# Optimization experiments

Hardware: AMD Instinct MI355X
Metric: run time of the kernel (lower is better)

The kernel has to match this reference:

```python
import jax, jax.numpy as jnp
import numpy as np

B, P, G = 16, 4096, 512          # images, proposals/image, gt boxes/image
NUM_CLASSES = 80
IOU_THRESH = 0.5                  # cfg.MODEL.ROI_HEADS.IOU_THRESHOLDS = [0.5]
BATCH_PER_IMG = 512               # cfg.MODEL.ROI_HEADS.BATCH_SIZE_PER_IMAGE
POS_FRAC = 0.25                   # cfg.MODEL.ROI_HEADS.POSITIVE_FRACTION
NUM_FG = int(BATCH_PER_IMG * POS_FRAC)   # 128
NUM_BG = BATCH_PER_IMG - NUM_FG          # 384
NEG_INF = jnp.float32(-1e9)


def _make_boxes(key, b, n, img_size=1024.0):
    # valid xyxy boxes inside an img_size x img_size image
    p = jax.random.uniform(key, (b, n, 4)) * img_size
    x1 = jnp.minimum(p[..., 0], p[..., 2]); x2 = jnp.maximum(p[..., 0], p[..., 2]) + 1.0
    y1 = jnp.minimum(p[..., 1], p[..., 3]); y2 = jnp.maximum(p[..., 1], p[..., 3]) + 1.0
    return jnp.stack([x1, y1, x2, y2], axis=-1)


def setup_inputs() -> dict:
    key = jax.random.key(0)
    k1, k2, k3, k4 = jax.random.split(key, 4)
    return {
        'proposal_boxes': _make_boxes(k1, B, P),
        'target_boxes': _make_boxes(k2, B, G),
        'gt_classes': jax.random.randint(k3, (B, G), 0, NUM_CLASSES),
        'priorities': jax.random.uniform(k4, (B, P)),  # random sampling keys (replaces tf random subsample)
    }


def _pairwise_iou(t, p):
    # t: [B,G,4] gt boxes, p: [B,P,4] proposals, xyxy -> iou [B,G,P]
    area_t = (t[..., 2] - t[..., 0]) * (t[..., 3] - t[..., 1])   # [B,G]
    area_p = (p[..., 2] - p[..., 0]) * (p[..., 3] - p[..., 1])   # [B,P]
    lt = jnp.maximum(t[:, :, None, :2], p[:, None, :, :2])       # [B,G,P,2]
    rb = jnp.minimum(t[:, :, None, 2:], p[:, None, :, 2:])       # [B,G,P,2]
    wh = jnp.clip(rb - lt, 0.0)
    inter = wh[..., 0] * wh[..., 1]                               # [B,G,P]
    union = area_t[:, :, None] + area_p[:, None, :] - inter
    return jnp.where(inter > 0, inter / jnp.maximum(union, 1e-8), 0.0)


def reference(proposal_boxes, target_boxes, gt_classes, priorities):
    # ---- Matcher: pairwise IoU + argmax over gt (thresholds [0.5], labels [0,1]) ----
    iou = _pairwise_iou(target_boxes, proposal_boxes)       # [B,G,P]
    matched_vals = iou.max(axis=1)                          # [B,P]
    matched_idxs = iou.argmax(axis=1)                       # [B,P]
    fg = matched_vals >= IOU_THRESH                         # label==1
    # gt_classes per proposal: matched class if fg, else background = num_classes
    cls_m = jnp.take_along_axis(gt_classes, matched_idxs, axis=1)
    prop_cls = jnp.where(fg, cls_m, NUM_CLASSES)            # [B,P]
    # ---- subsample_labels: pick up to NUM_FG fg and NUM_BG bg by random priority ----
    fg_sc = jnp.where(fg, priorities, NEG_INF)
    bg_sc = jnp.where(~fg, priorities, NEG_INF)
    fg_v, fg_i = jax.lax.top_k(fg_sc, NUM_FG)               # [B,NUM_FG]
    bg_v, bg_i = jax.lax.top_k(bg_sc, NUM_BG)               # [B,NUM_BG]
    inds = jnp.concatenate([fg_i, bg_i], axis=1)            # [B,S]
    valid = jnp.concatenate([fg_v, bg_v], axis=1) > NEG_INF / 2
    # ---- gather sampled proposals + assigned gt (pad_or_clip: zero invalid slots) ----
    s_boxes = jnp.take_along_axis(proposal_boxes, inds[..., None], axis=1)   # [B,S,4]
    s_midx = jnp.take_along_axis(matched_idxs, inds, axis=1)                  # [B,S]
    s_gt_boxes = jnp.take_along_axis(target_boxes, s_midx[..., None], axis=1) # [B,S,4]
    s_cls = jnp.where(valid, jnp.take_along_axis(prop_cls, inds, axis=1), -1) # [B,S]
    mask = valid[..., None].astype(s_boxes.dtype)
    out = jnp.concatenate([s_boxes, s_gt_boxes], axis=-1) * mask              # [B,S,8]
    return out, s_cls
```

## Files before the change

### kernel.cpp

```cpp
#include <hip/hip_runtime.h>
#include <stdint.h>

#define NB 16
#define NP 4096
#define NG 512
#define NCH 8
#define GC  (NG/NCH)
#define NCLS 80
#define KFG 128
#define KBG 384
#define NS 512
#define OUT_BOX (NB*NS*8)
#define OUT_CLS (NB*NS)
#define NBNP (NB*NP)
#define NBK 256

typedef unsigned long long u64;

__global__ __launch_bounds__(256) void k_match(
    const float4* __restrict__ prop,
    const float4* __restrict__ tgt,
    u64* __restrict__ pm)
{
    __shared__ float4 tb[GC];
    __shared__ float  ta[GC];

    const int tid  = threadIdx.x;
    const int bx   = blockIdx.x;
    const int c    = bx & (NCH - 1);
    const int pblk = (bx >> 3) & 15;
    const int b    = bx >> 7;

    if (tid < GC) {
        float4 t = tgt[b * NG + c * GC + tid];
        tb[tid] = t;
        ta[tid] = __fmul_rn(__fsub_rn(t.z, t.x), __fsub_rn(t.w, t.y));
    }
    __syncthreads();

    const int p = pblk * 256 + tid;
    const float4 pb = prop[b * NP + p];
    const float ap = __fmul_rn(__fsub_rn(pb.z, pb.x), __fsub_rn(pb.w, pb.y));

    float best = -1.0f;
    int   bi   = 0;
    #pragma unroll 4
    for (int g = 0; g < GC; ++g) {
        const float4 t = tb[g];
        const float ltx = fmaxf(t.x, pb.x);
        const float lty = fmaxf(t.y, pb.y);
        const float rbx = fminf(t.z, pb.z);
        const float rby = fminf(t.w, pb.w);
        const float w = fmaxf(__fsub_rn(rbx, ltx), 0.0f);
        const float h = fmaxf(__fsub_rn(rby, lty), 0.0f);
        const float inter = __fmul_rn(w, h);
        const float uni   = __fsub_rn(__fadd_rn(ta[g], ap), inter);
        if ((double)inter > (double)best * (double)uni) {
            const float iou = (inter > 0.0f)
                                ? __fdiv_rn(inter, fmaxf(uni, 1e-8f))
                                : 0.0f;
            if (iou > best) { best = iou; bi = g; }
        }
    }
    const int gg = c * GC + bi;
    pm[c * NBNP + b * NP + p] =
        ((u64)__float_as_uint(best) << 16) | (u64)(NG - 1 - gg);
}

__global__ __launch_bounds__(1024) void k_select(
    const float4* __restrict__ prop,
    const float4* __restrict__ tgt,
    const int*   __restrict__ gtc,
    const float* __restrict__ pri,
    const u64*   __restrict__ pm,
    float* __restrict__ out)
{
    __shared__ int cnt[2 * NBK];
    __shared__ int bsa[2 * NBK];
    __shared__ int cur[2 * NBK];
    __shared__ int sA[2 * NBK], sB[2 * NBK];
    __shared__ int s_tot0;
    __shared__ u64 gkeys[NP];

    const int tid = threadIdx.x;
    const int b   = blockIdx.x;

    float* oimg = out + (size_t)b * NS * 8;
    #pragma unroll
    for (int i = tid; i < NS * 8; i += 1024) oimg[i] = 0.0f;
    if (tid < NS) out[OUT_BOX + b * NS + tid] = -1.0f;

    if (tid < 2 * NBK) cnt[tid] = 0;
    __syncthreads();

    int mcat[4], mgrp[4], mmid[4];
    u64 mkey[4];
    #pragma unroll
    for (int t = 0; t < 4; ++t) {
        const int p = tid + t * 1024;
        const int idx = b * NP + p;
        u64 m = pm[idx];
        #pragma unroll
        for (int c = 1; c < NCH; ++c) {
            const u64 mc = pm[c * NBNP + idx];
            if (mc > m) m = mc;
        }
        const float best = __uint_as_float((unsigned)(m >> 16));
        mmid[t] = (NG - 1) - (int)(m & 0xFFFF);
        const int cat = (best >= 0.5f) ? 1 : 0;
        const float v = pri[idx];
        int bkt = (int)(v * 256.0f); if (bkt > 255) bkt = 255;
        mcat[t] = cat;
        mgrp[t] = cat * NBK + bkt;
        mkey[t] = ((u64)__float_as_uint(v) << 12) | (u64)(NP - 1 - p);
        atomicAdd(&cnt[mgrp[t]], 1);
    }
    __syncthreads();

    if (tid < 2 * NBK) sA[tid] = cnt[(tid & 256) | (255 - (tid & 255))];
    __syncthreads();

    int* pa = sA; int* pb2 = sB;
    for (int d = 1; d < 2 * NBK; d <<= 1) {
        if (tid < 2 * NBK) pb2[tid] = pa[tid] + ((tid >= d) ? pa[tid - d] : 0);
        __syncthreads();
        int* tmp = pa; pa = pb2; pb2 = tmp;
    }
    if (tid == 0) s_tot0 = pa[NBK - 1];
    if (tid < 2 * NBK) {
        const int grp = (tid & 256) | (255 - (tid & 255));
        const int excl = pa[tid] - cnt[grp];
        bsa[grp] = excl;
        cur[grp] = excl;
    }
    __syncthreads();

    #pragma unroll
    for (int t = 0; t < 4; ++t) {
        const int off = atomicAdd(&cur[mgrp[t]], 1);
        gkeys[off] = mkey[t];
    }
    __syncthreads();

    const int tot0 = s_tot0;
    #pragma unroll
    for (int t = 0; t < 4; ++t) {
        const int grp = mgrp[t];
        const int gs  = bsa[grp];
        const int gc  = cnt[grp];
        const u64 mine = mkey[t];
        int ahead = 0;
        for (int i = gs; i < gs + gc; ++i)
            ahead += (gkeys[i] > mine) ? 1 : 0;
        const int cat  = mcat[t];
        const int rank = (gs - (cat ? tot0 : 0)) + ahead;
        const int cap  = cat ? KFG : KBG;
        if (rank < cap) {
            const int p    = tid + t * 1024;
            const int slot = b * NS + (cat ? rank : KFG + rank);
            const float4 pb4 = prop[b * NP + p];
            const int    mi  = mmid[t];
            const float4 tb4 = tgt[b * NG + mi];
            float4* orow = (float4*)(out + (size_t)slot * 8);
            orow[0] = pb4;
            orow[1] = tb4;
            out[OUT_BOX + slot] = cat ? (float)gtc[b * NG + mi] : (float)NCLS;
        }
    }
}

extern "C" void kernel_launch(void* const* d_in, const int* in_sizes, int n_in,
                              void* d_out, int out_size, void* d_ws, size_t ws_size,
                              hipStream_t stream) {
    const float4* prop = (const float4*)d_in[0];
    const float4* tgt  = (const float4*)d_in[1];
    const int*    gtc  = (const int*)  d_in[2];
    const float*  pri  = (const float*)d_in[3];
    float* out = (float*)d_out;

    u64* pm = (u64*)d_ws;

    k_match<<<NB * 16 * NCH, 256, 0, stream>>>(prop, tgt, pm);
    k_select<<<NB, 1024, 0, stream>>>(prop, tgt, gtc, pri, pm, out);
}
```

Measured before the change: 48.27 us.

## Split per-image selection across 16 blocks and move output init into match kernel

The selection kernel previously ran one 1024-thread block per image (16 blocks total). Now each image gets 16 blocks of 512 threads. Every block redundantly rebuilds the bucket histogram and sorted key array, then ranks only its own 256-proposal chunk, so the GPU has more blocks to schedule. Output zero/-1 initialization moves into the match kernel. The double-precision early-out comparison in the IoU loop is replaced with a float comparison that has a small relative slack. The costs are redundant histogram work per block and reliance on the float slack to stay conservative.

```diff
diff --git a/kernel.cpp b/kernel.cpp
--- a/kernel.cpp
+++ b/kernel.cpp
@@ -14,13 +14,17 @@
 #define OUT_CLS (NB*NS)
 #define NBNP (NB*NP)
 #define NBK 256
+#define NGRP (2*NBK)
+#define RBLK 16
+#define CHK (NP/RBLK)
 
 typedef unsigned long long u64;
 
 __global__ __launch_bounds__(256) void k_match(
     const float4* __restrict__ prop,
     const float4* __restrict__ tgt,
-    u64* __restrict__ pm)
+    u64* __restrict__ pm,
+    float* __restrict__ out)
 {
     __shared__ float4 tb[GC];
     __shared__ float  ta[GC];
@@ -30,6 +34,10 @@
     const int c    = bx & (NCH - 1);
     const int pblk = (bx >> 3) & 15;
     const int b    = bx >> 7;
+
+    const int gid = bx * 256 + tid;
+    if (gid < OUT_BOX) out[gid] = 0.0f;
+    if (gid < OUT_CLS) out[OUT_BOX + gid] = -1.0f;
 
     if (tid < GC) {
         float4 t = tgt[b * NG + c * GC + tid];
@@ -55,7 +63,9 @@
         const float h = fmaxf(__fsub_rn(rby, lty), 0.0f);
         const float inter = __fmul_rn(w, h);
         const float uni   = __fsub_rn(__fadd_rn(ta[g], ap), inter);
-        if ((double)inter > (double)best * (double)uni) {
+        const float tt = __fmul_rn(best, uni);
+        const float ss = fmaf(tt, -0x1p-23f, tt);
+        if (inter > ss) {
             const float iou = (inter > 0.0f)
                                 ? __fdiv_rn(inter, fmaxf(uni, 1e-8f))
                                 : 0.0f;
@@ -67,7 +77,7 @@
         ((u64)__float_as_uint(best) << 16) | (u64)(NG - 1 - gg);
 }
 
-__global__ __launch_bounds__(1024) void k_select(
+__global__ __launch_bounds__(512) void k_rank(
     const float4* __restrict__ prop,
     const float4* __restrict__ tgt,
     const int*   __restrict__ gtc,
@@ -75,29 +85,24 @@
     const u64*   __restrict__ pm,
     float* __restrict__ out)
 {
-    __shared__ int cnt[2 * NBK];
-    __shared__ int bsa[2 * NBK];
-    __shared__ int cur[2 * NBK];
-    __shared__ int sA[2 * NBK], sB[2 * NBK];
+    __shared__ u64 gkeys[NP];
+    __shared__ int cnt[NGRP];
+    __shared__ int bsa[NGRP];
+    __shared__ int cur[NGRP];
+    __shared__ int sA[NGRP], sB[NGRP];
     __shared__ int s_tot0;
-    __shared__ u64 gkeys[NP];
 
     const int tid = threadIdx.x;
-    const int b   = blockIdx.x;
+    const int b   = blockIdx.x >> 4;
+    const int j   = blockIdx.x & (RBLK - 1);
 
-    float* oimg = out + (size_t)b * NS * 8;
-    #pragma unroll
-    for (int i = tid; i < NS * 8; i += 1024) oimg[i] = 0.0f;
-    if (tid < NS) out[OUT_BOX + b * NS + tid] = -1.0f;
-
-    if (tid < 2 * NBK) cnt[tid] = 0;
+    cnt[tid] = 0;
     __syncthreads();
 
-    int mcat[4], mgrp[4], mmid[4];
-    u64 mkey[4];
+    u64 skey[8]; short sgrp[8];
     #pragma unroll
-    for (int t = 0; t < 4; ++t) {
-        const int p = tid + t * 1024;
+    for (int t = 0; t < 8; ++t) {
+        const int p = tid + t * 512;
         const int idx = b * NP + p;
         u64 m = pm[idx];
         #pragma unroll
@@ -106,28 +111,27 @@
             if (mc > m) m = mc;
         }
         const float best = __uint_as_float((unsigned)(m >> 16));
-        mmid[t] = (NG - 1) - (int)(m & 0xFFFF);
         const int cat = (best >= 0.5f) ? 1 : 0;
         const float v = pri[idx];
         int bkt = (int)(v * 256.0f); if (bkt > 255) bkt = 255;
-        mcat[t] = cat;
-        mgrp[t] = cat * NBK + bkt;
-        mkey[t] = ((u64)__float_as_uint(v) << 12) | (u64)(NP - 1 - p);
-        atomicAdd(&cnt[mgrp[t]], 1);
+        const int grp = cat * NBK + bkt;
+        skey[t] = ((u64)__float_as_uint(v) << 12) | (u64)(NP - 1 - p);
+        sgrp[t] = (short)grp;
+        atomicAdd(&cnt[grp], 1);
     }
     __syncthreads();
 
-    if (tid < 2 * NBK) sA[tid] = cnt[(tid & 256) | (255 - (tid & 255))];
+    sA[tid] = cnt[(tid & 256) | (255 - (tid & 255))];
     __syncthreads();
 
     int* pa = sA; int* pb2 = sB;
-    for (int d = 1; d < 2 * NBK; d <<= 1) {
-        if (tid < 2 * NBK) pb2[tid] = pa[tid] + ((tid >= d) ? pa[tid - d] : 0);
+    for (int d = 1; d < NGRP; d <<= 1) {
+        pb2[tid] = pa[tid] + ((tid >= d) ? pa[tid - d] : 0);
         __syncthreads();
         int* tmp = pa; pa = pb2; pb2 = tmp;
     }
     if (tid == 0) s_tot0 = pa[NBK - 1];
-    if (tid < 2 * NBK) {
+    {
         const int grp = (tid & 256) | (255 - (tid & 255));
         const int excl = pa[tid] - cnt[grp];
         bsa[grp] = excl;
@@ -136,30 +140,39 @@
     __syncthreads();
 
     #pragma unroll
-    for (int t = 0; t < 4; ++t) {
-        const int off = atomicAdd(&cur[mgrp[t]], 1);
-        gkeys[off] = mkey[t];
+    for (int t = 0; t < 8; ++t) {
+        const int off = atomicAdd(&cur[(int)sgrp[t]], 1);
+        gkeys[off] = skey[t];
     }
     __syncthreads();
 
-    const int tot0 = s_tot0;
-    #pragma unroll
-    for (int t = 0; t < 4; ++t) {
-        const int grp = mgrp[t];
-        const int gs  = bsa[grp];
-        const int gc  = cnt[grp];
-        const u64 mine = mkey[t];
+    if (tid < CHK) {
+        const int p   = j * CHK + tid;
+        const int idx = b * NP + p;
+        u64 m = pm[idx];
+        #pragma unroll
+        for (int c = 1; c < NCH; ++c) {
+            const u64 mc = pm[c * NBNP + idx];
+            if (mc > m) m = mc;
+        }
+        const float best = __uint_as_float((unsigned)(m >> 16));
+        const int   mi   = (NG - 1) - (int)(m & 0xFFFF);
+        const int   cat  = (best >= 0.5f) ? 1 : 0;
+        const float v    = pri[idx];
+        int bkt = (int)(v * 256.0f); if (bkt > 255) bkt = 255;
+        const int grp = cat * NBK + bkt;
+        const u64 mine = ((u64)__float_as_uint(v) << 12) | (u64)(NP - 1 - p);
+
+        const int gs = bsa[grp];
+        const int gc = cnt[grp];
         int ahead = 0;
         for (int i = gs; i < gs + gc; ++i)
             ahead += (gkeys[i] > mine) ? 1 : 0;
-        const int cat  = mcat[t];
-        const int rank = (gs - (cat ? tot0 : 0)) + ahead;
+        const int rank = (gs - (cat ? s_tot0 : 0)) + ahead;
         const int cap  = cat ? KFG : KBG;
         if (rank < cap) {
-            const int p    = tid + t * 1024;
             const int slot = b * NS + (cat ? rank : KFG + rank);
-            const float4 pb4 = prop[b * NP + p];
-            const int    mi  = mmid[t];
+            const float4 pb4 = prop[idx];
             const float4 tb4 = tgt[b * NG + mi];
             float4* orow = (float4*)(out + (size_t)slot * 8);
             orow[0] = pb4;
@@ -180,6 +193,6 @@
 
     u64* pm = (u64*)d_ws;
 
-    k_match<<<NB * 16 * NCH, 256, 0, stream>>>(prop, tgt, pm);
-    k_select<<<NB, 1024, 0, stream>>>(prop, tgt, gtc, pri, pm, out);
+    k_match<<<NB * 16 * NCH, 256, 0, stream>>>(prop, tgt, pm, out);
+    k_rank<<<NB * RBLK, 512, 0, stream>>>(prop, tgt, gtc, pri, pm, out);
 }
```

Measured after the change: 46.88 us. 1.03x faster.
